# Kernel tuning notes

Hardware: AMD Instinct MI355X
Metric: run time of the kernel (lower is better)

Reference implementation:

```python
import jax, jax.numpy as jnp
import numpy as np


def setup_inputs() -> dict:
    key = jax.random.key(0)
    rain_hr = jax.random.normal(key, (16, 8, 1, 512, 512), dtype=jnp.float32)
    return {"rain_hr": rain_hr}


def reference(rain_hr):
    B, T, C, H, W = rain_hr.shape
    rain_mean = rain_hr.mean(axis=1)              # [B, C, H, W]

    fft = jnp.fft.fft2(rain_mean)                 # complex [B, C, H, W]
    power = jnp.abs(fft) ** 2                     # [B, C, H, W]

    # Integer radius map (torch: sqrt(...).long() truncates toward zero)
    ch, cw = H // 2, W // 2
    y = jnp.arange(H, dtype=jnp.float32) - ch
    x = jnp.arange(W, dtype=jnp.float32) - cw
    radius = jnp.sqrt(x[None, :] ** 2 + y[:, None] ** 2).astype(jnp.int32)  # [H, W]

    max_radius = min(H, W) // 2

    # power[..., mask].mean() == sum over (B, C, pixels at radius r) / (B*C*count_r)
    power_hw = power.sum(axis=(0, 1))             # [H, W]
    flat_r = radius.ravel()
    # out-of-range radii (>= max_radius) are dropped by segment_sum
    seg_sum = jax.ops.segment_sum(power_hw.ravel(), flat_r, num_segments=max_radius)
    counts = jax.ops.segment_sum(jnp.ones((H * W,), jnp.float32), flat_r, num_segments=max_radius)

    cnt = counts[1:]                               # radii 1 .. max_radius-1
    denom = jnp.maximum(cnt, 1.0) * (B * C)
    gen_spectrum = jnp.where(cnt > 0, seg_sum[1:] / denom, 0.0)

    k = jnp.arange(1, max_radius, dtype=jnp.float32)
    ref = k ** (-5.0 / 3.0)
    ref = ref / (ref.sum() + 1e-8)

    gen_norm = gen_spectrum / (gen_spectrum.sum() + 1e-8)
    loss = jnp.mean((gen_norm - ref) ** 2)
    return loss
```

## Files before the change

kernel.cpp:

```cpp
#include <hip/hip_runtime.h>
#include <math.h>

#define N 512
#define PLANE ((size_t)N * N)
#define NEG2PI (-6.28318530717958647692f)

__device__ inline void dft8(float (&xr)[8], float (&xi)[8]) {
    const float S = 0.70710678118654752440f;
    float t0r = xr[0] + xr[4], t0i = xi[0] + xi[4];
    float t4r = xr[0] - xr[4], t4i = xi[0] - xi[4];
    float t1r = xr[1] + xr[5], t1i = xi[1] + xi[5];
    float t5r = xr[1] - xr[5], t5i = xi[1] - xi[5];
    float t2r = xr[2] + xr[6], t2i = xi[2] + xi[6];
    float t6r = xr[2] - xr[6], t6i = xi[2] - xi[6];
    float t3r = xr[3] + xr[7], t3i = xi[3] + xi[7];
    float t7r = xr[3] - xr[7], t7i = xi[3] - xi[7];
    float o1r = S * (t5r + t5i), o1i = S * (t5i - t5r);
    float o2r = t6i,             o2i = -t6r;
    float o3r = S * (t7i - t7r), o3i = -S * (t7r + t7i);
    float p0r = t0r + t2r, p0i = t0i + t2i;
    float p1r = t1r + t3r, p1i = t1i + t3i;
    float q0r = t0r - t2r, q0i = t0i - t2i;
    float q1r = t1i - t3i, q1i = -(t1r - t3r);
    xr[0] = p0r + p1r; xi[0] = p0i + p1i;
    xr[4] = p0r - p1r; xi[4] = p0i - p1i;
    xr[2] = q0r + q1r; xi[2] = q0i + q1i;
    xr[6] = q0r - q1r; xi[6] = q0i - q1i;
    float r0r = t4r + o2r, r0i = t4i + o2i;
    float r1r = o1r + o3r, r1i = o1i + o3i;
    float u0r = t4r - o2r, u0i = t4i - o2i;
    float u1r = o1i - o3i, u1i = -(o1r - o3r);
    xr[1] = r0r + r1r; xi[1] = r0i + r1i;
    xr[5] = r0r - r1r; xi[5] = r0i - r1i;
    xr[3] = u0r + u1r; xi[3] = u0i + u1i;
    xr[7] = u0r - u1r; xi[7] = u0i - u1i;
}

__device__ inline void twiddle_apply(float (&xr)[8], float (&xi)[8], float ang1) {
    float ts = __sinf(ang1), tc = __cosf(ang1);
    float wr = tc, wi = ts;
    #pragma unroll
    for (int k = 1; k < 8; ++k) {
        float nr = xr[k] * wr - xi[k] * wi;
        float ni = xr[k] * wi + xi[k] * wr;
        xr[k] = nr; xi[k] = ni;
        float w2r = wr * tc - wi * ts;
        float w2i = wr * ts + wi * tc;
        wr = w2r; wi = w2i;
    }
}

__device__ inline void fft512_wave(float (&xr)[8], float (&xi)[8],
                                   float* sre, float* sim, const int l) {
    dft8(xr, xi);
    twiddle_apply(xr, xi, (NEG2PI / 512.0f) * (float)l);
    const int w0 = l + (l >> 3);
    #pragma unroll
    for (int k = 0; k < 8; ++k) { sre[72 * k + w0] = xr[k]; sim[72 * k + w0] = xi[k]; }
    const int i2 = l & 7;
    const int rbase = 72 * (l >> 3) + i2;
    #pragma unroll
    for (int q = 0; q < 8; ++q) { xr[q] = sre[rbase + 9 * q]; xi[q] = sim[rbase + 9 * q]; }
    dft8(xr, xi);
    twiddle_apply(xr, xi, (NEG2PI / 64.0f) * (float)i2);
    #pragma unroll
    for (int k = 0; k < 8; ++k) { sre[rbase + 9 * k] = xr[k]; sim[rbase + 9 * k] = xi[k]; }
    const int r3 = 9 * l;
    #pragma unroll
    for (int q = 0; q < 8; ++q) { xr[q] = sre[r3 + q]; xi[q] = sim[r3 + q]; }
    dft8(xr, xi);
}

__global__ __launch_bounds__(256, 4) void kern_rowfft(const float* __restrict__ in,
                                                      float2* __restrict__ ws,
                                                      float* __restrict__ bins) {
    __shared__ float sRe[4][576];
    __shared__ float sIm[4][576];
    const int b   = blockIdx.x;
    const int j   = b & 7;
    const int sub = b >> 3;
    const int wv  = threadIdx.x >> 6;
    const int l   = threadIdx.x & 63;
    const int y   = sub * 4 + wv;
    if (b == 0) {
        #pragma unroll
        for (int i = 0; i < 9; ++i) bins[i * 256 + threadIdx.x] = 0.f;
    }
    const float* baseA = in + ((size_t)j * 8) * PLANE + (size_t)y * N;
    const float* baseB = in + ((size_t)(j + 8) * 8) * PLANE + (size_t)y * N;
    float* re = sRe[wv];
    float* im = sIm[wv];
    #pragma unroll
    for (int c0 = 0; c0 < 2; ++c0) {
        const int c = l + 64 * c0;
        float4 va[8], vb[8];
        #pragma unroll
        for (int tt = 0; tt < 8; ++tt) va[tt] = *(const float4*)(baseA + tt * PLANE + 4 * c);
        #pragma unroll
        for (int tt = 0; tt < 8; ++tt) vb[tt] = *(const float4*)(baseB + tt * PLANE + 4 * c);
        float4 sa, sb;
        sa.x = ((va[0].x + va[1].x) + (va[2].x + va[3].x)) + ((va[4].x + va[5].x) + (va[6].x + va[7].x));
        sa.y = ((va[0].y + va[1].y) + (va[2].y + va[3].y)) + ((va[4].y + va[5].y) + (va[6].y + va[7].y));
        sa.z = ((va[0].z + va[1].z) + (va[2].z + va[3].z)) + ((va[4].z + va[5].z) + (va[6].z + va[7].z));
        sa.w = ((va[0].w + va[1].w) + (va[2].w + va[3].w)) + ((va[4].w + va[5].w) + (va[6].w + va[7].w));
        sb.x = ((vb[0].x + vb[1].x) + (vb[2].x + vb[3].x)) + ((vb[4].x + vb[5].x) + (vb[6].x + vb[7].x));
        sb.y = ((vb[0].y + vb[1].y) + (vb[2].y + vb[3].y)) + ((vb[4].y + vb[5].y) + (vb[6].y + vb[7].y));
        sb.z = ((vb[0].z + vb[1].z) + (vb[2].z + vb[3].z)) + ((vb[4].z + vb[5].z) + (vb[6].z + vb[7].z));
        sb.w = ((vb[0].w + vb[1].w) + (vb[2].w + vb[3].w)) + ((vb[4].w + vb[5].w) + (vb[6].w + vb[7].w));
        const int i0 = 4 * c;
        const int p0 = i0 + (i0 >> 3);
        re[p0 + 0] = sa.x * 0.125f; re[p0 + 1] = sa.y * 0.125f;
        re[p0 + 2] = sa.z * 0.125f; re[p0 + 3] = sa.w * 0.125f;
        im[p0 + 0] = sb.x * 0.125f; im[p0 + 1] = sb.y * 0.125f;
        im[p0 + 2] = sb.z * 0.125f; im[p0 + 3] = sb.w * 0.125f;
    }
    float xr[8], xi[8];
    #pragma unroll
    for (int q = 0; q < 8; ++q) {
        const int p = l + (l >> 3) + 72 * q;
        xr[q] = re[p]; xi[q] = im[p];
    }
    fft512_wave(xr, xi, re, im, l);
    float2* wp = ws + ((size_t)j << 18) + ((size_t)y << 9);
    #pragma unroll
    for (int k = 0; k < 8; ++k) {
        wp[64 * k + 8 * (l & 7) + (l >> 3)] = make_float2(xr[k], xi[k]);
    }
}

__global__ __launch_bounds__(512, 4) void kern_colfft(const float2* __restrict__ ws,
                                                      float* __restrict__ gseg,
                                                      float* __restrict__ gcnt) {
    __shared__ float sA[8 * 576];
    __shared__ float sB[8 * 576];
    __shared__ float lseg[256];
    __shared__ float lcnt[256];
    const int b   = blockIdx.x;
    const int j   = b & 7;
    const int sub = b >> 3;
    const int fx0 = sub * 8;
    const int t   = threadIdx.x;
    const int w   = t >> 6;
    const int l   = t & 63;
    if (t < 256) { lseg[t] = 0.f; lcnt[t] = 0.f; }
    const float2* base = ws + ((size_t)j << 18) + fx0;
    #pragma unroll
    for (int i = 0; i < 8; ++i) {
        const int y = (w << 6) + (i << 3) + (l >> 3);
        const int f = l & 7;
        float2 v = base[((size_t)y << 9) + f];
        sA[y * 9 + f] = v.x;
        sB[y * 9 + f] = v.y;
    }
    __syncthreads();
    float xr[8], xi[8];
    #pragma unroll
    for (int q = 0; q < 8; ++q) {
        const int y = l + (q << 6);
        xr[q] = sA[y * 9 + w];
        xi[q] = sB[y * 9 + w];
    }
    __syncthreads();
    fft512_wave(xr, xi, sA + w * 576, sB + w * 576, l);
    const int dx  = fx0 + w - 256;
    const int dx2 = dx * dx;
    #pragma unroll
    for (int k = 0; k < 8; ++k) {
        const int fy = 64 * k + 8 * (l & 7) + (l >> 3);
        const int dy = fy - 256;
        const int d2 = dx2 + dy * dy;
        int r = (int)sqrtf((float)d2);
        if ((r + 1) * (r + 1) <= d2) r++;
        else if (r * r > d2) r--;
        if (r >= 1 && r < 256) {
            atomicAdd(&lseg[r], xr[k] * xr[k] + xi[k] * xi[k]);
            if (j == 0) atomicAdd(&lcnt[r], 1.0f);
        }
    }
    __syncthreads();
    if (t < 256) {
        if (lseg[t] != 0.f) atomicAdd(&gseg[j * 256 + t], lseg[t]);
    } else if (j == 0) {
        if (lcnt[t - 256] != 0.f) atomicAdd(&gcnt[t - 256], lcnt[t - 256]);
    }
}

__global__ __launch_bounds__(256) void kern_loss(const float* __restrict__ gseg,
                                                 const float* __restrict__ gcnt,
                                                 float* __restrict__ out) {
    __shared__ float red[256];
    const int t = threadIdx.x;
    float gen = 0.f, refv = 0.f;
    if (t >= 1) {
        float s = 0.f;
        #pragma unroll
        for (int jj = 0; jj < 8; ++jj) s += gseg[jj * 256 + t];
        float c = gcnt[t];
        gen  = (c > 0.f) ? s / (fmaxf(c, 1.f) * 16.0f) : 0.f;
        refv = exp2f(-1.66666666667f * log2f((float)t));
    }
    red[t] = gen; __syncthreads();
    for (int off = 128; off > 0; off >>= 1) {
        if (t < off) red[t] += red[t + off];
        __syncthreads();
    }
    const float sgen = red[0]; __syncthreads();
    red[t] = refv; __syncthreads();
    for (int off = 128; off > 0; off >>= 1) {
        if (t < off) red[t] += red[t + off];
        __syncthreads();
    }
    const float sref = red[0]; __syncthreads();
    const float gn = gen  / (sgen + 1e-8f);
    const float rn = refv / (sref + 1e-8f);
    red[t] = (gn - rn) * (gn - rn); __syncthreads();
    for (int off = 128; off > 0; off >>= 1) {
        if (t < off) red[t] += red[t + off];
        __syncthreads();
    }
    if (t == 0) out[0] = red[0] / 255.0f;
}

extern "C" void kernel_launch(void* const* d_in, const int* in_sizes, int n_in,
                              void* d_out, int out_size, void* d_ws, size_t ws_size,
                              hipStream_t stream) {
    const float* in = (const float*)d_in[0];
    float2* planes = (float2*)d_ws;
    float* bins = (float*)((char*)d_ws + (size_t)8 * N * N * sizeof(float2));
    float* gseg = bins;
    float* gcnt = bins + 8 * 256;
    kern_rowfft<<<1024, 256, 0, stream>>>(in, planes, bins);
    kern_colfft<<<512, 512, 0, stream>>>(planes, gseg, gcnt);
    kern_loss<<<1, 256, 0, stream>>>(gseg, gcnt, (float*)d_out);
}
```

Measured before the change: 216.6 us.

## Split temporal mean into a separate kernel before the row FFT

```diff
diff --git a/kernel.cpp b/kernel.cpp
--- a/kernel.cpp
+++ b/kernel.cpp
@@ -71,7 +71,39 @@
     dft8(xr, xi);
 }
 
-__global__ __launch_bounds__(256, 4) void kern_rowfft(const float* __restrict__ in,
+__global__ __launch_bounds__(256, 6) void kern_mean(const float* __restrict__ in,
+                                                    float2* __restrict__ mb) {
+    const int g = blockIdx.x * 256 + threadIdx.x;
+    const int c = g & 127;
+    const int y = (g >> 7) & 511;
+    const int j = g >> 16;
+    const float* pa = in + ((size_t)j * 8) * PLANE + (size_t)y * N + 4 * c;
+    const float* pb = in + ((size_t)(j + 8) * 8) * PLANE + (size_t)y * N + 4 * c;
+    float4 va[8], vb[8];
+    #pragma unroll
+    for (int tt = 0; tt < 8; ++tt) va[tt] = *(const float4*)(pa + tt * PLANE);
+    #pragma unroll
+    for (int tt = 0; tt < 8; ++tt) vb[tt] = *(const float4*)(pb + tt * PLANE);
+    float4 sa, sb;
+    sa.x = ((va[0].x + va[1].x) + (va[2].x + va[3].x)) + ((va[4].x + va[5].x) + (va[6].x + va[7].x));
+    sa.y = ((va[0].y + va[1].y) + (va[2].y + va[3].y)) + ((va[4].y + va[5].y) + (va[6].y + va[7].y));
+    sa.z = ((va[0].z + va[1].z) + (va[2].z + va[3].z)) + ((va[4].z + va[5].z) + (va[6].z + va[7].z));
+    sa.w = ((va[0].w + va[1].w) + (va[2].w + va[3].w)) + ((va[4].w + va[5].w) + (va[6].w + va[7].w));
+    sb.x = ((vb[0].x + vb[1].x) + (vb[2].x + vb[3].x)) + ((vb[4].x + vb[5].x) + (vb[6].x + vb[7].x));
+    sb.y = ((vb[0].y + vb[1].y) + (vb[2].y + vb[3].y)) + ((vb[4].y + vb[5].y) + (vb[6].y + vb[7].y));
+    sb.z = ((vb[0].z + vb[1].z) + (vb[2].z + vb[3].z)) + ((vb[4].z + vb[5].z) + (vb[6].z + vb[7].z));
+    sb.w = ((vb[0].w + vb[1].w) + (vb[2].w + vb[3].w)) + ((vb[4].w + vb[5].w) + (vb[6].w + vb[7].w));
+    float2* op = mb + ((size_t)j << 18) + ((size_t)y << 9) + 4 * c;
+    float4 o0, o1;
+    o0.x = sa.x * 0.125f; o0.y = sb.x * 0.125f;
+    o0.z = sa.y * 0.125f; o0.w = sb.y * 0.125f;
+    o1.x = sa.z * 0.125f; o1.y = sb.z * 0.125f;
+    o1.z = sa.w * 0.125f; o1.w = sb.w * 0.125f;
+    *(float4*)(op)     = o0;
+    *(float4*)(op + 2) = o1;
+}
+
+__global__ __launch_bounds__(256, 4) void kern_rowfft(const float2* __restrict__ mb,
                                                       float2* __restrict__ ws,
                                                       float* __restrict__ bins) {
     __shared__ float sRe[4][576];
@@ -86,41 +118,14 @@
         #pragma unroll
         for (int i = 0; i < 9; ++i) bins[i * 256 + threadIdx.x] = 0.f;
     }
-    const float* baseA = in + ((size_t)j * 8) * PLANE + (size_t)y * N;
-    const float* baseB = in + ((size_t)(j + 8) * 8) * PLANE + (size_t)y * N;
-    float* re = sRe[wv];
-    float* im = sIm[wv];
-    #pragma unroll
-    for (int c0 = 0; c0 < 2; ++c0) {
-        const int c = l + 64 * c0;
-        float4 va[8], vb[8];
-        #pragma unroll
-        for (int tt = 0; tt < 8; ++tt) va[tt] = *(const float4*)(baseA + tt * PLANE + 4 * c);
-        #pragma unroll
-        for (int tt = 0; tt < 8; ++tt) vb[tt] = *(const float4*)(baseB + tt * PLANE + 4 * c);
-        float4 sa, sb;
-        sa.x = ((va[0].x + va[1].x) + (va[2].x + va[3].x)) + ((va[4].x + va[5].x) + (va[6].x + va[7].x));
-        sa.y = ((va[0].y + va[1].y) + (va[2].y + va[3].y)) + ((va[4].y + va[5].y) + (va[6].y + va[7].y));
-        sa.z = ((va[0].z + va[1].z) + (va[2].z + va[3].z)) + ((va[4].z + va[5].z) + (va[6].z + va[7].z));
-        sa.w = ((va[0].w + va[1].w) + (va[2].w + va[3].w)) + ((va[4].w + va[5].w) + (va[6].w + va[7].w));
-        sb.x = ((vb[0].x + vb[1].x) + (vb[2].x + vb[3].x)) + ((vb[4].x + vb[5].x) + (vb[6].x + vb[7].x));
-        sb.y = ((vb[0].y + vb[1].y) + (vb[2].y + vb[3].y)) + ((vb[4].y + vb[5].y) + (vb[6].y + vb[7].y));
-        sb.z = ((vb[0].z + vb[1].z) + (vb[2].z + vb[3].z)) + ((vb[4].z + vb[5].z) + (vb[6].z + vb[7].z));
-        sb.w = ((vb[0].w + vb[1].w) + (vb[2].w + vb[3].w)) + ((vb[4].w + vb[5].w) + (vb[6].w + vb[7].w));
-        const int i0 = 4 * c;
-        const int p0 = i0 + (i0 >> 3);
-        re[p0 + 0] = sa.x * 0.125f; re[p0 + 1] = sa.y * 0.125f;
-        re[p0 + 2] = sa.z * 0.125f; re[p0 + 3] = sa.w * 0.125f;
-        im[p0 + 0] = sb.x * 0.125f; im[p0 + 1] = sb.y * 0.125f;
-        im[p0 + 2] = sb.z * 0.125f; im[p0 + 3] = sb.w * 0.125f;
-    }
+    const float2* rp = mb + ((size_t)j << 18) + ((size_t)y << 9);
+    float2 v[8];
+    #pragma unroll
+    for (int q = 0; q < 8; ++q) v[q] = rp[l + 64 * q];
     float xr[8], xi[8];
     #pragma unroll
-    for (int q = 0; q < 8; ++q) {
-        const int p = l + (l >> 3) + 72 * q;
-        xr[q] = re[p]; xi[q] = im[p];
-    }
-    fft512_wave(xr, xi, re, im, l);
+    for (int q = 0; q < 8; ++q) { xr[q] = v[q].x; xi[q] = v[q].y; }
+    fft512_wave(xr, xi, sRe[wv], sIm[wv], l);
     float2* wp = ws + ((size_t)j << 18) + ((size_t)y << 9);
     #pragma unroll
     for (int k = 0; k < 8; ++k) {
@@ -225,11 +230,13 @@
                               void* d_out, int out_size, void* d_ws, size_t ws_size,
                               hipStream_t stream) {
     const float* in = (const float*)d_in[0];
-    float2* planes = (float2*)d_ws;
-    float* bins = (float*)((char*)d_ws + (size_t)8 * N * N * sizeof(float2));
+    float2* mb     = (float2*)d_ws;
+    float2* planes = (float2*)((char*)d_ws + (size_t)8 * N * N * sizeof(float2));
+    float* bins = (float*)((char*)d_ws + (size_t)16 * N * N * sizeof(float2));
     float* gseg = bins;
     float* gcnt = bins + 8 * 256;
-    kern_rowfft<<<1024, 256, 0, stream>>>(in, planes, bins);
+    kern_mean<<<2048, 256, 0, stream>>>(in, mb);
+    kern_rowfft<<<1024, 256, 0, stream>>>(mb, planes, bins);
     kern_colfft<<<512, 512, 0, stream>>>(planes, gseg, gcnt);
     kern_loss<<<1, 256, 0, stream>>>(gseg, gcnt, (float*)d_out);
 }
```

After: 220.4 us. About the same (+1.8%).
